# Performance work log

Measured on AMD Instinct MI355X. Metric: run time of the kernel, lower is better.

## Reference

```python
import jax, jax.numpy as jnp
import numpy as np

T = 4            # number of node types (len(output_sizes))
N = 16384        # nodes per type
D_IN = 512       # input_size
D_H = 1024       # hidden_size
OUT_SIZES = (128, 96, 64, 32)
MAX_OUT = max(OUT_SIZES)


def setup_inputs() -> dict:
    key = jax.random.key(0)
    ks = jax.random.split(key, 16)
    inp = {}
    for t in range(T):
        inp[f"x{t}"] = jax.random.normal(ks[t], (N, D_IN), jnp.float32)
    # nodes are grouped by type (sorted), matching the padded dict layout
    inp["node_type"] = jnp.repeat(jnp.arange(T, dtype=jnp.int64), N)
    # layer1: per-type Linear(input_size, hidden_size) (apply_net)
    inp["W1"] = jax.random.normal(ks[4], (T, D_IN, D_H), jnp.float32) * 0.02
    inp["b1"] = jnp.zeros((T, D_H), jnp.float32)
    # layer2: per-type Linear(hidden_size, out_size_t)
    for t in range(T):
        inp[f"W2_{t}"] = jax.random.normal(ks[5 + t], (D_H, OUT_SIZES[t]), jnp.float32) * 0.02
        inp[f"b2_{t}"] = jnp.zeros((OUT_SIZES[t],), jnp.float32)
    return inp


def reference(x0, x1, x2, x3, node_type, W1, b1,
              W2_0, b2_0, W2_1, b2_1, W2_2, b2_2, W2_3, b2_3):
    # Per-type gather is implicit: x{t} already holds the features of the
    # nodes whose node_type == t (node_type is sorted/blocked).
    xs = jnp.stack([x0, x1, x2, x3])                       # [T, N, D_IN]
    # apply_net: layer1 per type + activation (batched grouped-GEMM)
    h = jax.nn.relu(jnp.einsum('tni,tih->tnh', xs, W1) + b1[:, None, :])  # [T, N, D_H]
    W2s = (W2_0, W2_1, W2_2, W2_3)
    b2s = (b2_0, b2_1, b2_2, b2_3)
    outs = []
    for t in range(T):  # fixed small set of structurally distinct heads
        o = h[t] @ W2s[t] + b2s[t]                         # [N, out_t]
        outs.append(jnp.pad(o, ((0, 0), (0, MAX_OUT - o.shape[1]))))  # _pad to MAX_OUT
    return jnp.stack(outs)                                 # [T, N, MAX_OUT]
```

## Files before the change

kernel.cpp:

```cpp
#include <hip/hip_runtime.h>
#include <hip/hip_bf16.h>


typedef __attribute__((ext_vector_type(8))) short short8;
typedef __attribute__((ext_vector_type(4))) float f32x4;

#define NT 4
#define NNODE 16384
#define DIN 512
#define DH 1024
#define MAXO 128

static __device__ __forceinline__ ushort f2bf(float f) {
    __hip_bfloat16 h = __float2bfloat16(f);
    return *reinterpret_cast<ushort*>(&h);
}

#define GLD(gsrc, ldst)                                                        \
    __builtin_amdgcn_global_load_lds(                                          \
        (const __attribute__((address_space(1))) void*)(gsrc),                 \
        (__attribute__((address_space(3))) void*)(ldst), 16, 0, 0)

__global__ __launch_bounds__(256) void cvt_x_kernel(
    const float* __restrict__ x0, const float* __restrict__ x1,
    const float* __restrict__ x2, const float* __restrict__ x3,
    ushort* __restrict__ out) {
    const int i = blockIdx.x * 256 + threadIdx.x;
    const int per_t = (NNODE * DIN) / 8;
    const int t = i >> 20;
    const int loc = i & (per_t - 1);
    const float* x = (t == 0) ? x0 : (t == 1) ? x1 : (t == 2) ? x2 : x3;
    const float4* xv = reinterpret_cast<const float4*>(x) + (size_t)loc * 2;
    float4 a = xv[0], b = xv[1];
    union { short8 v; ushort u[8]; } r;
    float f[8] = {a.x, a.y, a.z, a.w, b.x, b.y, b.z, b.w};
#pragma unroll
    for (int j = 0; j < 8; ++j) r.u[j] = f2bf(f[j]);
    reinterpret_cast<short8*>(out)[i] = r.v;
}

__global__ __launch_bounds__(256) void cvt_w_t_kernel(
    const float* __restrict__ in, ushort* __restrict__ out,
    int R, int Cin, size_t in_tstride, size_t out_tstride) {
    __shared__ float tile[32][33];
    const int t = blockIdx.z;
    in += (size_t)t * in_tstride;
    out += (size_t)t * out_tstride;
    const int c0 = blockIdx.x * 32, r0 = blockIdx.y * 32;
    const int cx = threadIdx.x & 31;
    const int ry = threadIdx.x >> 5;
#pragma unroll
    for (int j = 0; j < 4; ++j) {
        int rr = ry + j * 8;
        int c = c0 + cx;
        tile[rr][cx] = (c < Cin) ? in[(size_t)(r0 + rr) * Cin + c] : 0.0f;
    }
    __syncthreads();
#pragma unroll
    for (int j = 0; j < 4; ++j) {
        int cc = ry + j * 8;
        out[(size_t)(c0 + cc) * R + r0 + cx] = f2bf(tile[cx][cc]);
    }
}

__global__ void pad_b2_kernel(const float* __restrict__ b0, const float* __restrict__ b1,
                              const float* __restrict__ b2, const float* __restrict__ b3,
                              float* __restrict__ out) {
    const int i = threadIdx.x;
    const int t = i >> 7, n = i & 127;
    const int sz[4] = {128, 96, 64, 32};
    const float* b = (t == 0) ? b0 : (t == 1) ? b1 : (t == 2) ? b2 : b3;
    out[i] = (n < sz[t]) ? b[n] : 0.0f;
}

template <int BN, bool RELU, bool OUTBF16>
__global__ __launch_bounds__(512, 1) void gemm1b(
    const ushort* __restrict__ Abase, const ushort* __restrict__ Bbase,
    const float* __restrict__ biasbase, void* __restrict__ Cbase,
    int N, int K, int MT,
    size_t strideA, size_t strideB, size_t strideBias, size_t strideC) {
    constexpr int NF = BN / 64;
    constexpr int NBC = BN * 8 / 512;
    constexpr int ABYTES = 256 * 64 * 2;
    constexpr int BBYTES = BN * 64 * 2;
    constexpr int BUF = ABYTES + BBYTES;
    __shared__ char lds[2 * BUF];

    const int cpx = gridDim.x >> 3;
    const int g = blockIdx.x;
    const int wg = (g & 7) * cpx + (g >> 3);
    const int NTL = N / BN;
    const int t = wg / (MT * NTL);
    const int rmn = wg % (MT * NTL);
    const int m0 = (rmn / NTL) * 256;
    const int n0 = (rmn % NTL) * BN;

    const ushort* A = Abase + (size_t)t * strideA;
    const ushort* Bp = Bbase + (size_t)t * strideB;
    const float* bias = biasbase + (size_t)t * strideBias;

    const int tid = threadIdx.x;
    const int lane = tid & 63;
    const int w = tid >> 6;
    const int wm = w >> 2, wn = w & 3;
    const int lrow = lane & 15, lgrp = lane >> 4;

    const ushort* asrc[4];
    int adst[4];
#pragma unroll
    for (int j = 0; j < 4; ++j) {
        const int c = j * 512 + tid;
        const int r = c >> 3;
        const int cb = ((c & 7) * 16) ^ ((r & 7) << 4);
        asrc[j] = A + (size_t)(m0 + r) * K + (cb >> 1);
        adst[j] = c * 16;
    }
    const ushort* bsrc[NBC];
    int bdst[NBC];
#pragma unroll
    for (int j = 0; j < NBC; ++j) {
        const int c = j * 512 + tid;
        const int r = c >> 3;
        const int cb = ((c & 7) * 16) ^ ((r & 7) << 4);
        bsrc[j] = Bp + (size_t)(n0 + r) * K + (cb >> 1);
        bdst[j] = ABYTES + c * 16;
    }

    f32x4 acc[8][NF] = {};
    const int NK = K / 64;

#pragma unroll
    for (int j = 0; j < 4; ++j) GLD(asrc[j], lds + adst[j]);
#pragma unroll
    for (int j = 0; j < NBC; ++j) GLD(bsrc[j], lds + bdst[j]);
    asm volatile("s_waitcnt vmcnt(0)" ::: "memory");
    __builtin_amdgcn_s_barrier();
    asm volatile("" ::: "memory");

    for (int i = 0; i < NK; ++i) {
        const char* cu_ = lds + (i & 1) * BUF;
        char* nx_ = lds + ((i + 1) & 1) * BUF;
        const int ktn = (i + 1) * 64;
        const bool st = (i + 1 < NK);

        if (st) {
#pragma unroll
            for (int j = 0; j < 4; ++j) GLD(asrc[j] + ktn, nx_ + adst[j]);
#pragma unroll
            for (int j = 0; j < NBC; ++j) GLD(bsrc[j] + ktn, nx_ + bdst[j]);
        }

#pragma unroll
        for (int kkk = 0; kkk < 2; ++kkk) {
            short8 bfr[NF], af[8];
#pragma unroll
            for (int ni = 0; ni < NF; ++ni) {
                const int br = wn * (NF * 16) + ni * 16 + lrow;
                const int kb = (kkk * 64 + lgrp * 16) ^ ((br & 7) << 4);
                bfr[ni] = *(const short8*)(cu_ + ABYTES + br * 128 + kb);
            }
#pragma unroll
            for (int ml = 0; ml < 8; ++ml) {
                const int ar = wm * 128 + ml * 16 + lrow;
                const int kb = (kkk * 64 + lgrp * 16) ^ ((ar & 7) << 4);
                af[ml] = *(const short8*)(cu_ + ar * 128 + kb);
            }
#pragma unroll
            for (int ml = 0; ml < 8; ++ml)
#pragma unroll
                for (int ni = 0; ni < NF; ++ni)
                    acc[ml][ni] = __builtin_amdgcn_mfma_f32_16x16x32_bf16(
                        bfr[ni], af[ml], acc[ml][ni], 0, 0, 0);
        }

        if (st) {
            asm volatile("s_waitcnt vmcnt(0)" ::: "memory");
            __builtin_amdgcn_s_barrier();
            asm volatile("" ::: "memory");
        }
    }

    const int wnoff = n0 + wn * (NF * 16);
    const int wmoff = m0 + wm * 128;
#pragma unroll
    for (int ni = 0; ni < NF; ++ni) {
        const int ncol = wnoff + ni * 16 + lgrp * 4;
        const float4 bv = *reinterpret_cast<const float4*>(&bias[ncol]);
#pragma unroll
        for (int mi = 0; mi < 8; ++mi) {
            const int row = wmoff + mi * 16 + lrow;
            float v0 = acc[mi][ni][0] + bv.x;
            float v1 = acc[mi][ni][1] + bv.y;
            float v2 = acc[mi][ni][2] + bv.z;
            float v3 = acc[mi][ni][3] + bv.w;
            if (RELU) {
                v0 = fmaxf(v0, 0.0f); v1 = fmaxf(v1, 0.0f);
                v2 = fmaxf(v2, 0.0f); v3 = fmaxf(v3, 0.0f);
            }
            const size_t base = (size_t)t * strideC + (size_t)row * N + ncol;
            if (OUTBF16) {
                uint2 p;
                p.x = (uint)f2bf(v0) | ((uint)f2bf(v1) << 16);
                p.y = (uint)f2bf(v2) | ((uint)f2bf(v3) << 16);
                *reinterpret_cast<uint2*>(&((ushort*)Cbase)[base]) = p;
            } else {
                float4 p = {v0, v1, v2, v3};
                *reinterpret_cast<float4*>(&((float*)Cbase)[base]) = p;
            }
        }
    }
}

extern "C" void kernel_launch(void* const* d_in, const int* in_sizes, int n_in,
                              void* d_out, int out_size, void* d_ws, size_t ws_size,
                              hipStream_t stream) {
    const float* x0 = (const float*)d_in[0];
    const float* x1 = (const float*)d_in[1];
    const float* x2 = (const float*)d_in[2];
    const float* x3 = (const float*)d_in[3];
    const float* W1 = (const float*)d_in[5];
    const float* b1 = (const float*)d_in[6];
    const float* W2[4] = {(const float*)d_in[7], (const float*)d_in[9],
                          (const float*)d_in[11], (const float*)d_in[13]};
    const float* b2[4] = {(const float*)d_in[8], (const float*)d_in[10],
                          (const float*)d_in[12], (const float*)d_in[14]};

    char* ws = (char*)d_ws;
    ushort* H   = (ushort*)ws;
    ushort* Xbf = (ushort*)(ws + 134217728ull);
    ushort* W1T = (ushort*)(ws + 134217728ull + 67108864ull);
    ushort* W2T = (ushort*)(ws + 134217728ull + 67108864ull + 4194304ull);
    float*  b2p = (float*)(ws + 134217728ull + 67108864ull + 4194304ull + 1048576ull);

    cvt_x_kernel<<<16384, 256, 0, stream>>>(x0, x1, x2, x3, Xbf);
    cvt_w_t_kernel<<<dim3(32, 16, 4), 256, 0, stream>>>(
        W1, W1T, DIN, DH, (size_t)DIN * DH, (size_t)DH * DIN);
    const int osz[4] = {128, 96, 64, 32};
    for (int t = 0; t < 4; ++t)
        cvt_w_t_kernel<<<dim3(4, 32, 1), 256, 0, stream>>>(
            W2[t], W2T + (size_t)t * MAXO * DH, DH, osz[t], 0, 0);
    pad_b2_kernel<<<1, 512, 0, stream>>>(b2[0], b2[1], b2[2], b2[3], b2p);

    gemm1b<256, true, true><<<1024, 512, 0, stream>>>(
        Xbf, W1T, b1, H,
        DH, DIN, NNODE / 256,
        (size_t)NNODE * DIN, (size_t)DH * DIN, (size_t)DH, (size_t)NNODE * DH);

    gemm1b<128, false, false><<<256, 512, 0, stream>>>(
        H, W2T, b2p, d_out,
        MAXO, DH, NNODE / 256,
        (size_t)NNODE * DH, (size_t)MAXO * DH, (size_t)MAXO, (size_t)NNODE * MAXO);
}
```

Baseline: 185.7 us.

## Fuse fp32-to-bf16 input conversion into GEMM1 and switch to 128x128 tiles

Removes the separate X conversion kernel. GEMM1 now loads fp32 activations straight into registers, packs them to bf16 and writes them to swizzled LDS, while B still uses direct global-to-LDS loads. Both GEMMs move to 128x128 tiles with 256 threads and two blocks per CU. This avoids writing and re-reading a 64MB bf16 copy of X, but GEMM1 reads fp32 A (twice the bytes per tile) through register staging, and the smaller tiles cut per-block data reuse.

```diff
diff --git a/kernel.cpp b/kernel.cpp
--- a/kernel.cpp
+++ b/kernel.cpp
@@ -16,28 +16,17 @@
     return *reinterpret_cast<ushort*>(&h);
 }
 
+static __device__ __forceinline__ short8 pack8(const float4 a, const float4 b) {
+    union { short8 v; ushort u[8]; } r;
+    r.u[0] = f2bf(a.x); r.u[1] = f2bf(a.y); r.u[2] = f2bf(a.z); r.u[3] = f2bf(a.w);
+    r.u[4] = f2bf(b.x); r.u[5] = f2bf(b.y); r.u[6] = f2bf(b.z); r.u[7] = f2bf(b.w);
+    return r.v;
+}
+
 #define GLD(gsrc, ldst)                                                        \
     __builtin_amdgcn_global_load_lds(                                          \
         (const __attribute__((address_space(1))) void*)(gsrc),                 \
         (__attribute__((address_space(3))) void*)(ldst), 16, 0, 0)
-
-__global__ __launch_bounds__(256) void cvt_x_kernel(
-    const float* __restrict__ x0, const float* __restrict__ x1,
-    const float* __restrict__ x2, const float* __restrict__ x3,
-    ushort* __restrict__ out) {
-    const int i = blockIdx.x * 256 + threadIdx.x;
-    const int per_t = (NNODE * DIN) / 8;
-    const int t = i >> 20;
-    const int loc = i & (per_t - 1);
-    const float* x = (t == 0) ? x0 : (t == 1) ? x1 : (t == 2) ? x2 : x3;
-    const float4* xv = reinterpret_cast<const float4*>(x) + (size_t)loc * 2;
-    float4 a = xv[0], b = xv[1];
-    union { short8 v; ushort u[8]; } r;
-    float f[8] = {a.x, a.y, a.z, a.w, b.x, b.y, b.z, b.w};
-#pragma unroll
-    for (int j = 0; j < 8; ++j) r.u[j] = f2bf(f[j]);
-    reinterpret_cast<short8*>(out)[i] = r.v;
-}
 
 __global__ __launch_bounds__(256) void cvt_w_t_kernel(
     const float* __restrict__ in, ushort* __restrict__ out,
@@ -73,67 +62,82 @@
     out[i] = (n < sz[t]) ? b[n] : 0.0f;
 }
 
-template <int BN, bool RELU, bool OUTBF16>
-__global__ __launch_bounds__(512, 1) void gemm1b(
-    const ushort* __restrict__ Abase, const ushort* __restrict__ Bbase,
-    const float* __restrict__ biasbase, void* __restrict__ Cbase,
-    int N, int K, int MT,
+template <bool AFP32, bool RELU, bool OUTBF16>
+__global__ __launch_bounds__(256, 2) void gemm128(
+    const void* __restrict__ A0, const void* __restrict__ A1,
+    const void* __restrict__ A2, const void* __restrict__ A3,
+    const ushort* __restrict__ Bbase, const float* __restrict__ biasbase,
+    void* __restrict__ Cbase, int N, int K, int MT,
     size_t strideA, size_t strideB, size_t strideBias, size_t strideC) {
-    constexpr int NF = BN / 64;
-    constexpr int NBC = BN * 8 / 512;
-    constexpr int ABYTES = 256 * 64 * 2;
-    constexpr int BBYTES = BN * 64 * 2;
-    constexpr int BUF = ABYTES + BBYTES;
+    constexpr int ABY = 128 * 64 * 2;
+    constexpr int BBY = 128 * 64 * 2;
+    constexpr int BUF = ABY + BBY;
     __shared__ char lds[2 * BUF];
 
     const int cpx = gridDim.x >> 3;
     const int g = blockIdx.x;
     const int wg = (g & 7) * cpx + (g >> 3);
-    const int NTL = N / BN;
+    const int NTL = N / 128;
     const int t = wg / (MT * NTL);
     const int rmn = wg % (MT * NTL);
-    const int m0 = (rmn / NTL) * 256;
-    const int n0 = (rmn % NTL) * BN;
-
-    const ushort* A = Abase + (size_t)t * strideA;
+    const int m0 = (rmn / NTL) * 128;
+    const int n0 = (rmn % NTL) * 128;
+
+    const float* Af = (const float*)((t == 0) ? A0 : (t == 1) ? A1
+                                   : (t == 2) ? A2 : A3);
+    const ushort* Ab = (const ushort*)A0 + (size_t)t * strideA;
     const ushort* Bp = Bbase + (size_t)t * strideB;
     const float* bias = biasbase + (size_t)t * strideBias;
 
     const int tid = threadIdx.x;
     const int lane = tid & 63;
     const int w = tid >> 6;
-    const int wm = w >> 2, wn = w & 3;
+    const int wm = w >> 1, wn = w & 1;
     const int lrow = lane & 15, lgrp = lane >> 4;
 
-    const ushort* asrc[4];
-    int adst[4];
+    const float* af32src[4];
+    const ushort* abfsrc[4];
+    const ushort* bsrc[4];
+    int adst[4], bdst[4];
 #pragma unroll
     for (int j = 0; j < 4; ++j) {
-        const int c = j * 512 + tid;
+        const int c = j * 256 + tid;
         const int r = c >> 3;
-        const int cb = ((c & 7) * 16) ^ ((r & 7) << 4);
-        asrc[j] = A + (size_t)(m0 + r) * K + (cb >> 1);
-        adst[j] = c * 16;
-    }
-    const ushort* bsrc[NBC];
-    int bdst[NBC];
-#pragma unroll
-    for (int j = 0; j < NBC; ++j) {
-        const int c = j * 512 + tid;
-        const int r = c >> 3;
-        const int cb = ((c & 7) * 16) ^ ((r & 7) << 4);
+        const int c8 = c & 7;
+        const int cb = (c8 * 16) ^ ((r & 7) << 4);
+        if (AFP32) {
+            af32src[j] = Af + (size_t)(m0 + r) * K + c8 * 8;
+            adst[j] = r * 128 + cb;
+        } else {
+            abfsrc[j] = Ab + (size_t)(m0 + r) * K + (cb >> 1);
+            adst[j] = c * 16;
+        }
         bsrc[j] = Bp + (size_t)(n0 + r) * K + (cb >> 1);
-        bdst[j] = ABYTES + c * 16;
-    }
-
-    f32x4 acc[8][NF] = {};
+        bdst[j] = ABY + c * 16;
+    }
+
+    f32x4 acc[4][4] = {};
     const int NK = K / 64;
-
-#pragma unroll
-    for (int j = 0; j < 4; ++j) GLD(asrc[j], lds + adst[j]);
-#pragma unroll
-    for (int j = 0; j < NBC; ++j) GLD(bsrc[j], lds + bdst[j]);
-    asm volatile("s_waitcnt vmcnt(0)" ::: "memory");
+    float4 fa[4][2];
+
+    if (AFP32) {
+#pragma unroll
+        for (int j = 0; j < 4; ++j) {
+            fa[j][0] = *reinterpret_cast<const float4*>(af32src[j]);
+            fa[j][1] = *reinterpret_cast<const float4*>(af32src[j] + 4);
+        }
+#pragma unroll
+        for (int j = 0; j < 4; ++j) GLD(bsrc[j], lds + bdst[j]);
+#pragma unroll
+        for (int j = 0; j < 4; ++j)
+            *reinterpret_cast<short8*>(lds + adst[j]) = pack8(fa[j][0], fa[j][1]);
+    } else {
+#pragma unroll
+        for (int j = 0; j < 4; ++j) GLD(abfsrc[j], lds + adst[j]);
+#pragma unroll
+        for (int j = 0; j < 4; ++j) GLD(bsrc[j], lds + bdst[j]);
+    }
+    asm volatile("s_waitcnt vmcnt(0) lgkmcnt(0)" ::: "memory");
     __builtin_amdgcn_s_barrier();
     asm volatile("" ::: "memory");
 
@@ -144,50 +148,64 @@
         const bool st = (i + 1 < NK);
 
         if (st) {
-#pragma unroll
-            for (int j = 0; j < 4; ++j) GLD(asrc[j] + ktn, nx_ + adst[j]);
-#pragma unroll
-            for (int j = 0; j < NBC; ++j) GLD(bsrc[j] + ktn, nx_ + bdst[j]);
+            if (AFP32) {
+#pragma unroll
+                for (int j = 0; j < 4; ++j) {
+                    fa[j][0] = *reinterpret_cast<const float4*>(af32src[j] + ktn);
+                    fa[j][1] = *reinterpret_cast<const float4*>(af32src[j] + ktn + 4);
+                }
+            } else {
+#pragma unroll
+                for (int j = 0; j < 4; ++j) GLD(abfsrc[j] + ktn, nx_ + adst[j]);
+            }
+#pragma unroll
+            for (int j = 0; j < 4; ++j) GLD(bsrc[j] + ktn, nx_ + bdst[j]);
         }
 
 #pragma unroll
         for (int kkk = 0; kkk < 2; ++kkk) {
-            short8 bfr[NF], af[8];
-#pragma unroll
-            for (int ni = 0; ni < NF; ++ni) {
-                const int br = wn * (NF * 16) + ni * 16 + lrow;
+            short8 bfr[4], af[4];
+#pragma unroll
+            for (int ni = 0; ni < 4; ++ni) {
+                const int br = wn * 64 + ni * 16 + lrow;
                 const int kb = (kkk * 64 + lgrp * 16) ^ ((br & 7) << 4);
-                bfr[ni] = *(const short8*)(cu_ + ABYTES + br * 128 + kb);
-            }
-#pragma unroll
-            for (int ml = 0; ml < 8; ++ml) {
-                const int ar = wm * 128 + ml * 16 + lrow;
+                bfr[ni] = *(const short8*)(cu_ + ABY + br * 128 + kb);
+            }
+#pragma unroll
+            for (int ml = 0; ml < 4; ++ml) {
+                const int ar = wm * 64 + ml * 16 + lrow;
                 const int kb = (kkk * 64 + lgrp * 16) ^ ((ar & 7) << 4);
                 af[ml] = *(const short8*)(cu_ + ar * 128 + kb);
             }
 #pragma unroll
-            for (int ml = 0; ml < 8; ++ml)
-#pragma unroll
-                for (int ni = 0; ni < NF; ++ni)
+            for (int ml = 0; ml < 4; ++ml)
+#pragma unroll
+                for (int ni = 0; ni < 4; ++ni)
                     acc[ml][ni] = __builtin_amdgcn_mfma_f32_16x16x32_bf16(
                         bfr[ni], af[ml], acc[ml][ni], 0, 0, 0);
         }
 
         if (st) {
-            asm volatile("s_waitcnt vmcnt(0)" ::: "memory");
+            if (AFP32) {
+#pragma unroll
+                for (int j = 0; j < 4; ++j)
+                    *reinterpret_cast<short8*>(nx_ + adst[j]) =
+                        pack8(fa[j][0], fa[j][1]);
+            }
+            asm volatile("s_waitcnt vmcnt(0) lgkmcnt(0)" ::: "memory");
             __builtin_amdgcn_s_barrier();
             asm volatile("" ::: "memory");
         }
     }
 
-    const int wnoff = n0 + wn * (NF * 16);
-    const int wmoff = m0 + wm * 128;
-#pragma unroll
-    for (int ni = 0; ni < NF; ++ni) {
+    const int wnoff = n0 + wn * 64;
+    const int wmoff = m0 + wm * 64;
+#pragma unroll
+    for (int ni = 0; ni < 4; ++ni) {
         const int ncol = wnoff + ni * 16 + lgrp * 4;
         const float4 bv = *reinterpret_cast<const float4*>(&bias[ncol]);
 #pragma unroll
-        for (int mi = 0; mi < 8; ++mi) {
+        for (int mi = 0; mi < 4; ++mi) {
             const int row = wmoff + mi * 16 + lrow;
             float v0 = acc[mi][ni][0] + bv.x;
             float v1 = acc[mi][ni][1] + bv.y;
@@ -227,12 +245,10 @@
 
     char* ws = (char*)d_ws;
     ushort* H   = (ushort*)ws;
-    ushort* Xbf = (ushort*)(ws + 134217728ull);
-    ushort* W1T = (ushort*)(ws + 134217728ull + 67108864ull);
-    ushort* W2T = (ushort*)(ws + 134217728ull + 67108864ull + 4194304ull);
-    float*  b2p = (float*)(ws + 134217728ull + 67108864ull + 4194304ull + 1048576ull);
-
-    cvt_x_kernel<<<16384, 256, 0, stream>>>(x0, x1, x2, x3, Xbf);
+    ushort* W1T = (ushort*)(ws + 134217728ull);
+    ushort* W2T = (ushort*)(ws + 134217728ull + 4194304ull);
+    float*  b2p = (float*)(ws + 134217728ull + 4194304ull + 1048576ull);
+
     cvt_w_t_kernel<<<dim3(32, 16, 4), 256, 0, stream>>>(
         W1, W1T, DIN, DH, (size_t)DIN * DH, (size_t)DH * DIN);
     const int osz[4] = {128, 96, 64, 32};
@@ -241,13 +257,14 @@
             W2[t], W2T + (size_t)t * MAXO * DH, DH, osz[t], 0, 0);
     pad_b2_kernel<<<1, 512, 0, stream>>>(b2[0], b2[1], b2[2], b2[3], b2p);
 
-    gemm1b<256, true, true><<<1024, 512, 0, stream>>>(
-        Xbf, W1T, b1, H,
-        DH, DIN, NNODE / 256,
-        (size_t)NNODE * DIN, (size_t)DH * DIN, (size_t)DH, (size_t)NNODE * DH);
-
-    gemm1b<128, false, false><<<256, 512, 0, stream>>>(
-        H, W2T, b2p, d_out,
-        MAXO, DH, NNODE / 256,
-        (size_t)NNODE * DH, (size_t)MAXO * DH, (size_t)MAXO, (size_t)NNODE * MAXO);
-}
+    gemm128<true, true, true><<<4096, 256, 0, stream>>>(
+        x0, x1, x2, x3, W1T, b1, H,
+        DH, DIN, NNODE / 128,
+        0, (size_t)DH * DIN, (size_t)DH, (size_t)NNODE * DH);
+
+    gemm128<false, false, false><<<512, 256, 0, stream>>>(
+        H, H, H, H, W2T, b2p, d_out,
+        MAXO, DH, NNODE / 128,
+        (size_t)NNODE * DH, (size_t)MAXO * DH, (size_t)MAXO,
+        (size_t)NNODE * MAXO);
+}
```

New measurement: 207.0 us. 1.11x slower.
